# Kernel optimization log

Hardware: AMD Instinct MI355X
Metric: run time of the kernel (lower is better)

The kernel has to match this reference:

```python
import jax, jax.numpy as jnp
import numpy as np

VOCAB, HIDDEN, POOL, NHASH = 32000, 256, 100000, 20


def setup_inputs() -> dict:
    key = jax.random.key(0)
    k1, k2, k3, k4 = jax.random.split(key, 4)
    x = jax.random.normal(k1, (2, 2048, HIDDEN), dtype=jnp.float32)
    pool = jax.random.normal(k2, (POOL, HIDDEN), dtype=jnp.float32)
    # original init is constant 1/num_hash; use rand to make gradients nontrivial,
    # scaled similarly
    import_params = jax.random.uniform(k3, (VOCAB, NHASH), dtype=jnp.float32) / NHASH
    hash_values = jax.random.randint(k4, (VOCAB, NHASH), 0, POOL, dtype=jnp.int64)
    return {"x": x, "pool": pool, "import_params": import_params, "hash_values": hash_values}


def reference(x, pool, import_params, hash_values):
    # gather hashed embeddings: [V, J, H]
    gathered = pool[hash_values]
    # weighted sum over hashes -> [V, H]
    embed = jnp.einsum('vj,vjh->vh', import_params, gathered)
    # logits: [..., V]
    return jnp.matmul(x, embed.T)
```

## Files before the change

kernel.cpp:

```cpp
#include <hip/hip_runtime.h>
#include <hip/hip_bf16.h>

#define VOCAB  32000
#define HIDDEN 256
#define NHASH  20
#define MROWS  4096
#define KDIM   256
#define POOL   100000
#define XBLK   1024

typedef __attribute__((ext_vector_type(8))) short bf16x8;
typedef __attribute__((ext_vector_type(8))) unsigned short u16x8;
typedef __attribute__((ext_vector_type(4))) float f32x4;

__device__ __forceinline__ unsigned short f32_bf16_rne(float f) {
  union { float f; unsigned int u; } v; v.f = f;
  unsigned int r = v.u + 0x7FFF + ((v.u >> 16) & 1);
  return (unsigned short)(r >> 16);
}

__device__ __forceinline__ float bf16_f32(unsigned short u) {
  union { unsigned int u; float f; } v; v.u = (unsigned int)u << 16;
  return v.f;
}

__device__ __forceinline__ void async16(const void* g, void* l) {
  __builtin_amdgcn_global_load_lds(
      (const __attribute__((address_space(1))) unsigned int*)g,
      (__attribute__((address_space(3))) unsigned int*)l, 16, 0, 0);
}

__device__ __forceinline__ ushort4 f4_to_bf4(float4 f) {
  ushort4 o;
  o.x = f32_bf16_rne(f.x); o.y = f32_bf16_rne(f.y);
  o.z = f32_bf16_rne(f.z); o.w = f32_bf16_rne(f.w);
  return o;
}

#define POOL_F4 (POOL * HIDDEN / 4)
#define X_F4    (MROWS * HIDDEN / 4)
__global__ __launch_bounds__(256)
void cast_kernel(const float* __restrict__ x, const float* __restrict__ pool,
                 unsigned short* __restrict__ xb, unsigned short* __restrict__ poolb) {
  const int step = gridDim.x * 256;
  for (int i = blockIdx.x * 256 + threadIdx.x; i < POOL_F4 + X_F4; i += step) {
    if (i < POOL_F4) {
      ((ushort4*)poolb)[i] = f4_to_bf4(((const float4*)pool)[i]);
    } else {
      const int j = i - POOL_F4;
      ((ushort4*)xb)[j] = f4_to_bf4(((const float4*)x)[j]);
    }
  }
}

__global__ __launch_bounds__(256)
void embed_kernel(const unsigned short* __restrict__ poolb,
                  const float* __restrict__ w, const int* __restrict__ hash,
                  unsigned short* __restrict__ eb) {
  const int v    = blockIdx.x * 4 + (threadIdx.x >> 6);
  const int lane = threadIdx.x & 63;
  const int half = lane >> 5;
  const int sub  = lane & 31;
  int   hl = 0; float wl = 0.f;
  if (lane < NHASH) {
    hl = hash[v * NHASH + lane];
    wl = w[v * NHASH + lane];
  }
  float acc[8] = {};
#pragma unroll
  for (int j = 0; j < NHASH; j += 2) {
    const int   h  = __shfl(hl, j + half);
    const float ww = __shfl(wl, j + half);
    const u16x8 p = *(const u16x8*)(poolb + (size_t)h * HIDDEN + sub * 8);
#pragma unroll
    for (int k = 0; k < 8; ++k) acc[k] += ww * bf16_f32(p[k]);
  }
#pragma unroll
  for (int k = 0; k < 8; ++k) acc[k] += __shfl_xor(acc[k], 32);
  if (lane < 32) {
    u16x8 o;
#pragma unroll
    for (int k = 0; k < 8; ++k) o[k] = f32_bf16_rne(acc[k]);
    *(u16x8*)(eb + (size_t)v * HIDDEN + sub * 8) = o;
  }
}

__global__ __launch_bounds__(256)
void prep_kernel(const float* __restrict__ x, const float* __restrict__ pool,
                 const float* __restrict__ w, const int* __restrict__ hash,
                 unsigned short* __restrict__ xb, unsigned short* __restrict__ eb) {
  const int tid = threadIdx.x;
  if (blockIdx.x < XBLK) {
    const int i = blockIdx.x * 256 + tid;
    ((ushort4*)xb)[i] = f4_to_bf4(((const float4*)x)[i]);
    return;
  }
  const int v    = (blockIdx.x - XBLK) * 4 + (tid >> 6);
  const int lane = tid & 63;
  int   hl = 0; float wl = 0.f;
  if (lane < NHASH) {
    hl = hash[v * NHASH + lane];
    wl = w[v * NHASH + lane];
  }
  float4 acc = make_float4(0.f, 0.f, 0.f, 0.f);
#pragma unroll
  for (int j = 0; j < NHASH; ++j) {
    const int   h  = __shfl(hl, j);
    const float ww = __shfl(wl, j);
    const float4 p = ((const float4*)(pool + (size_t)h * HIDDEN))[lane];
    acc.x += ww * p.x; acc.y += ww * p.y;
    acc.z += ww * p.z; acc.w += ww * p.w;
  }
  ((ushort4*)(eb + (size_t)v * HIDDEN))[lane] = f4_to_bf4(acc);
}

__global__ __launch_bounds__(256)
void gemm_kernel(const unsigned short* __restrict__ xb,
                 const unsigned short* __restrict__ eb,
                 float* __restrict__ out) {
  __shared__ char smem[32768] __attribute__((aligned(128)));
  short* As = (short*)smem;
  short* Bs = (short*)(smem + 16384);
  float* Cs = (float*)smem;

  const int tid  = threadIdx.x;
  const int lane = tid & 63;
  const int wave = tid >> 6;
  const int wm   = wave >> 1;
  const int wn   = wave & 1;

  const int bid  = blockIdx.x;
  const int swz  = (bid & 7) * 1000 + (bid >> 3);
  const int mtile = swz & 31;
  const int ntile = swz >> 5;
  const int mbase = mtile * 128;
  const int nbase = ntile * 128;

  int srow[4], scol[4];
#pragma unroll
  for (int i = 0; i < 4; ++i) {
    const int c = i * 256 + tid;
    srow[i] = c >> 3;
    scol[i] = (((c & 7) ^ ((c >> 3) & 7)) << 3);
  }

  f32x4 acc[4][4] = {};

  const int abase = (wm * 64 + (lane & 15)) * 128;
  const int bbase = (wn * 64 + (lane & 15)) * 128;
  const int sw    = (lane & 7) << 4;
  const int kq    = (lane >> 4) << 4;

#pragma unroll
  for (int kt = 0; kt < 4; ++kt) {
    const int k0 = kt * 64;
#pragma unroll
    for (int i = 0; i < 4; ++i) {
      const int c = i * 256 + tid;
      async16(xb + (size_t)(mbase + srow[i]) * KDIM + k0 + scol[i], &As[c * 8]);
      async16(eb + (size_t)(nbase + srow[i]) * KDIM + k0 + scol[i], &Bs[c * 8]);
    }
    __syncthreads();

    const char* A = (const char*)As;
    const char* B = (const char*)Bs;
#pragma unroll
    for (int kk = 0; kk < 2; ++kk) {
      const int koff = (kk * 64 + kq) ^ sw;
      bf16x8 a[4], b[4];
#pragma unroll
      for (int mi = 0; mi < 4; ++mi)
        a[mi] = *(const bf16x8*)(A + abase + mi * 2048 + koff);
#pragma unroll
      for (int ni = 0; ni < 4; ++ni)
        b[ni] = *(const bf16x8*)(B + bbase + ni * 2048 + koff);
#pragma unroll
      for (int mi = 0; mi < 4; ++mi)
#pragma unroll
        for (int ni = 0; ni < 4; ++ni)
          acc[mi][ni] = __builtin_amdgcn_mfma_f32_16x16x32_bf16(
              a[mi], b[ni], acc[mi][ni], 0, 0, 0);
    }
    __syncthreads();
  }

#pragma unroll
  for (int ph = 0; ph < 2; ++ph) {
    if (wm == ph) {
      const int crow0 = (lane >> 4) << 2;
      const int ccol  = wn * 64 + (lane & 15);
#pragma unroll
      for (int mi = 0; mi < 4; ++mi)
#pragma unroll
        for (int ni = 0; ni < 4; ++ni)
#pragma unroll
          for (int j = 0; j < 4; ++j)
            Cs[(crow0 + mi * 16 + j) * 128 + ccol + ni * 16] = acc[mi][ni][j];
    }
    __syncthreads();
#pragma unroll
    for (int i = 0; i < 8; ++i) {
      const int flat = i * 1024 + tid * 4;
      const int row  = flat >> 7;
      const int col  = flat & 127;
      f32x4 vv = *(const f32x4*)&Cs[row * 128 + col];
      __builtin_nontemporal_store(vv,
          (f32x4*)&out[(size_t)(mbase + ph * 64 + row) * VOCAB + nbase + col]);
    }
    if (ph == 0) __syncthreads();
  }
}

extern "C" void kernel_launch(void* const* d_in, const int* in_sizes, int n_in,
                              void* d_out, int out_size, void* d_ws, size_t ws_size,
                              hipStream_t stream) {
  const float* x    = (const float*)d_in[0];
  const float* pool = (const float*)d_in[1];
  const float* imp  = (const float*)d_in[2];
  const int*   hash = (const int*)d_in[3];
  float* out = (float*)d_out;

  unsigned short* xb    = (unsigned short*)d_ws;
  unsigned short* eb    = xb + (size_t)MROWS * HIDDEN;
  unsigned short* poolb = eb + (size_t)VOCAB * HIDDEN;

  const size_t need = ((size_t)MROWS + VOCAB + POOL) * HIDDEN * 2;
  if (ws_size >= need) {
    cast_kernel<<<2048, 256, 0, stream>>>(x, pool, xb, poolb);
    embed_kernel<<<VOCAB / 4, 256, 0, stream>>>(poolb, imp, hash, eb);
  } else {
    prep_kernel<<<XBLK + VOCAB / 4, 256, 0, stream>>>(x, pool, imp, hash, xb, eb);
  }
  gemm_kernel<<<(MROWS / 128) * (VOCAB / 128), 256, 0, stream>>>(xb, eb, out);
}
```

Before: 191.0 us.

## Double-buffer GEMM LDS tiles with K=32 steps to overlap loads and MFMA

Restructures the GEMM main loop from four single-buffered K=64 stages into eight K=32 stages over two LDS buffers. The next tile's async global-to-LDS loads are issued before computing on the current buffer, and the XOR swizzle is adapted to the 64-byte row layout. The aim is to hide global load latency behind MFMA work and drop one barrier per stage. In exchange there are more, smaller iterations, each ending in a barrier. The async loads may also not complete before use without an explicit vmcnt wait, since only __syncthreads guards them.

```diff
diff --git a/kernel.cpp b/kernel.cpp
--- a/kernel.cpp
+++ b/kernel.cpp
@@ -119,8 +119,6 @@
                  const unsigned short* __restrict__ eb,
                  float* __restrict__ out) {
   __shared__ char smem[32768] __attribute__((aligned(128)));
-  short* As = (short*)smem;
-  short* Bs = (short*)(smem + 16384);
   float* Cs = (float*)smem;
 
   const int tid  = threadIdx.x;
@@ -136,52 +134,60 @@
   const int mbase = mtile * 128;
   const int nbase = ntile * 128;
 
-  int srow[4], scol[4];
-#pragma unroll
-  for (int i = 0; i < 4; ++i) {
+  int srow[2], skoff[2];
+#pragma unroll
+  for (int i = 0; i < 2; ++i) {
     const int c = i * 256 + tid;
-    srow[i] = c >> 3;
-    scol[i] = (((c & 7) ^ ((c >> 3) & 7)) << 3);
+    srow[i]  = c >> 2;
+    skoff[i] = (((c & 3) ^ ((c >> 2) & 3)) << 3);
   }
 
   f32x4 acc[4][4] = {};
 
-  const int abase = (wm * 64 + (lane & 15)) * 128;
-  const int bbase = (wn * 64 + (lane & 15)) * 128;
-  const int sw    = (lane & 7) << 4;
-  const int kq    = (lane >> 4) << 4;
-
-#pragma unroll
-  for (int kt = 0; kt < 4; ++kt) {
-    const int k0 = kt * 64;
-#pragma unroll
-    for (int i = 0; i < 4; ++i) {
-      const int c = i * 256 + tid;
-      async16(xb + (size_t)(mbase + srow[i]) * KDIM + k0 + scol[i], &As[c * 8]);
-      async16(eb + (size_t)(nbase + srow[i]) * KDIM + k0 + scol[i], &Bs[c * 8]);
-    }
+  const int abase = (wm * 64 + (lane & 15)) * 64;
+  const int bbase = (wn * 64 + (lane & 15)) * 64;
+  const int rdoff = (((lane >> 4) ^ (lane & 3)) << 4);
+
+#pragma unroll
+  for (int i = 0; i < 2; ++i) {
+    const int c = i * 256 + tid;
+    async16(xb + (size_t)(mbase + srow[i]) * KDIM + skoff[i], smem + c * 16);
+    async16(eb + (size_t)(nbase + srow[i]) * KDIM + skoff[i], smem + 8192 + c * 16);
+  }
+  __syncthreads();
+
+  int buf = 0;
+#pragma unroll
+  for (int kt = 0; kt < 8; ++kt) {
+    if (kt < 7) {
+      const int nb = (buf ^ 1) * 16384;
+      const int k0 = (kt + 1) * 32;
+#pragma unroll
+      for (int i = 0; i < 2; ++i) {
+        const int c = i * 256 + tid;
+        async16(xb + (size_t)(mbase + srow[i]) * KDIM + k0 + skoff[i],
+                smem + nb + c * 16);
+        async16(eb + (size_t)(nbase + srow[i]) * KDIM + k0 + skoff[i],
+                smem + nb + 8192 + c * 16);
+      }
+    }
+    const char* A = (const char*)smem + buf * 16384;
+    const char* B = (const char*)smem + buf * 16384 + 8192;
+    bf16x8 a[4], b[4];
+#pragma unroll
+    for (int mi = 0; mi < 4; ++mi)
+      a[mi] = *(const bf16x8*)(A + abase + mi * 1024 + rdoff);
+#pragma unroll
+    for (int ni = 0; ni < 4; ++ni)
+      b[ni] = *(const bf16x8*)(B + bbase + ni * 1024 + rdoff);
+#pragma unroll
+    for (int mi = 0; mi < 4; ++mi)
+#pragma unroll
+      for (int ni = 0; ni < 4; ++ni)
+        acc[mi][ni] = __builtin_amdgcn_mfma_f32_16x16x32_bf16(
+            a[mi], b[ni], acc[mi][ni], 0, 0, 0);
     __syncthreads();
-
-    const char* A = (const char*)As;
-    const char* B = (const char*)Bs;
-#pragma unroll
-    for (int kk = 0; kk < 2; ++kk) {
-      const int koff = (kk * 64 + kq) ^ sw;
-      bf16x8 a[4], b[4];
-#pragma unroll
-      for (int mi = 0; mi < 4; ++mi)
-        a[mi] = *(const bf16x8*)(A + abase + mi * 2048 + koff);
-#pragma unroll
-      for (int ni = 0; ni < 4; ++ni)
-        b[ni] = *(const bf16x8*)(B + bbase + ni * 2048 + koff);
-#pragma unroll
-      for (int mi = 0; mi < 4; ++mi)
-#pragma unroll
-        for (int ni = 0; ni < 4; ++ni)
-          acc[mi][ni] = __builtin_amdgcn_mfma_f32_16x16x32_bf16(
-              a[mi], b[ni], acc[mi][ni], 0, 0, 0);
-    }
-    __syncthreads();
+    buf ^= 1;
   }
 
 #pragma unroll
```

Measured after the change: 204.4 us. +7.0%, slower.
